# Performance work log

Measured on AMD Instinct MI355X. Metric: run time of the kernel, lower is better.

Reference implementation:

```python
import jax, jax.numpy as jnp
import numpy as np

D = 1024
D_H = 64

def setup_inputs() -> dict:
    key = jax.random.key(0)
    kx, kq, kk, kv = jax.random.split(key, 4)
    B, T = 4, 4096
    x = jax.random.normal(kx, (B, T, D), dtype=jnp.float32)
    # nn.Linear(d, d_H, bias=False) weights, stored as [d, d_H] (already transposed)
    s = 1.0 / np.sqrt(D)
    Wq = jax.random.uniform(kq, (D, D_H), dtype=jnp.float32, minval=-s, maxval=s)
    Wk = jax.random.uniform(kk, (D, D_H), dtype=jnp.float32, minval=-s, maxval=s)
    Wv = jax.random.uniform(kv, (D, D_H), dtype=jnp.float32, minval=-s, maxval=s)
    return {"x": x, "Wq": Wq, "Wk": Wk, "Wv": Wv}

def reference(x, Wq, Wk, Wv):
    B, T, d = x.shape
    Q = jnp.einsum('btd,dh->bth', x, Wq)
    K = jnp.einsum('btd,dh->bth', x, Wk)
    V = jnp.einsum('btd,dh->bth', x, Wv)
    # NOTE: original scales by self.d ** -0.5 (model dim), not d_H
    scores = jnp.einsum('bqh,bkh->bqk', Q, K) * (d ** -0.5)
    causal = jnp.tril(jnp.ones((T, T), dtype=bool))  # [T, T]
    scores = jnp.where(causal, scores, -jnp.inf)
    attn = jax.nn.softmax(scores, axis=-1)
    return jnp.einsum('bqk,bkh->bqh', attn, V)
```

## Files before the change

### kernel.cpp

```cpp
#include <hip/hip_runtime.h>
#include <hip/hip_bf16.h>

#define D_MODEL 1024
#define D_HEAD  64
#define T_SEQ   4096
#define NB      4
#define NROWS   (NB * T_SEQ)
#define SPLIT   8

typedef float f32x4 __attribute__((ext_vector_type(4)));
typedef __bf16 bf16x8 __attribute__((ext_vector_type(8)));
typedef unsigned short u16;
typedef unsigned u32x2 __attribute__((ext_vector_type(2)));
typedef unsigned u32x4 __attribute__((ext_vector_type(4)));

__device__ inline unsigned pk_bf16(float a, float b) {
    unsigned ua = __builtin_bit_cast(unsigned, a);
    unsigned ub = __builtin_bit_cast(unsigned, b);
    ua = (ua + 0x7FFFu + ((ua >> 16) & 1u)) >> 16;
    ub = (ub + 0x7FFFu + ((ub >> 16) & 1u)) >> 16;
    return ua | (ub << 16);
}
__device__ inline u16 bf16r(float a) {
    unsigned ua = __builtin_bit_cast(unsigned, a);
    return (u16)((ua + 0x7FFFu + ((ua >> 16) & 1u)) >> 16);
}

__global__ __launch_bounds__(256) void packw_kernel(
    const float* __restrict__ Wq, const float* __restrict__ Wk,
    const float* __restrict__ Wv, unsigned* __restrict__ Wpk)
{
    const int id = blockIdx.x * 256 + threadIdx.x;
    const int kb = id / 192;
    const int n  = id - kb * 192;
    const int sel = n >> 6, col = n & 63;
    const float* W = sel == 0 ? Wq : (sel == 1 ? Wk : Wv);
    float f[8];
#pragma unroll
    for (int j = 0; j < 8; ++j) f[j] = W[(kb * 8 + j) * 64 + col];
    uint4 o;
    o.x = pk_bf16(f[0], f[1]); o.y = pk_bf16(f[2], f[3]);
    o.z = pk_bf16(f[4], f[5]); o.w = pk_bf16(f[6], f[7]);
    *(uint4*)(Wpk + (size_t)id * 4) = o;
}

__global__ __launch_bounds__(256) void qkv_kernel(
    const float* __restrict__ x, const unsigned* __restrict__ Wpk,
    u16* __restrict__ Qbf, u16* __restrict__ Kbf, u16* __restrict__ Vt)
{
    __shared__ __align__(16) unsigned Xs[2][16 * 68];
    __shared__ __align__(16) u16 Vbuf[64 * 16];

    const int tid  = threadIdx.x;
    const int w    = tid >> 6;
    const int lane = tid & 63;
    const int nl   = lane & 15;
    const int quad = lane >> 4;
    const long row0 = (long)blockIdx.x * 16;

    const int srow = tid >> 5;
    const int scol = (tid & 31) * 4;

    f32x4 acc[3] = {};

    f32x4 nx[2];
#pragma unroll
    for (int p = 0; p < 2; ++p)
        nx[p] = *(const f32x4*)(x + (row0 + p * 8 + srow) * D_MODEL + scol);

    for (int ch = 0; ch < 8; ++ch) {
        const int buf = ch & 1;
#pragma unroll
        for (int p = 0; p < 2; ++p) {
            uint2 pk2;
            pk2.x = pk_bf16(nx[p][0], nx[p][1]);
            pk2.y = pk_bf16(nx[p][2], nx[p][3]);
            *(uint2*)&Xs[buf][(p * 8 + srow) * 68 + (scol >> 1)] = pk2;
        }
        __syncthreads();
        if (ch < 7) {
#pragma unroll
            for (int p = 0; p < 2; ++p)
                nx[p] = *(const f32x4*)(x + (row0 + p * 8 + srow) * D_MODEL
                                          + (ch + 1) * 128 + scol);
        }
#pragma unroll
        for (int kk = 0; kk < 4; ++kk) {
            const bf16x8 a0 = __builtin_bit_cast(bf16x8,
                *(const uint4*)&Xs[buf][nl * 68 + kk * 16 + quad * 4]);
            const unsigned* wb = Wpk + (size_t)(ch * 16 + kk * 4 + quad) * 768
                                     + (w * 48 + nl) * 4;
#pragma unroll
            for (int t = 0; t < 3; ++t) {
                const bf16x8 b = __builtin_bit_cast(bf16x8, *(const uint4*)(wb + t * 64));
                acc[t] = __builtin_amdgcn_mfma_f32_16x16x32_bf16(a0, b, acc[t], 0, 0, 0);
            }
        }
    }
    __syncthreads();

    const float QSCALE = 0.04508422f;
#pragma unroll
    for (int t = 0; t < 3; ++t) {
        const int n0c = w * 48 + t * 16;
        const int sel = n0c >> 6;
        const int col = (n0c & 63) + nl;
        if (sel == 0) {
#pragma unroll
            for (int reg = 0; reg < 4; ++reg)
                Qbf[(row0 + quad * 4 + reg) * D_HEAD + col] =
                    bf16r(acc[t][reg] * QSCALE);
        } else if (sel == 1) {
#pragma unroll
            for (int reg = 0; reg < 4; ++reg)
                Kbf[(row0 + quad * 4 + reg) * D_HEAD + col] =
                    bf16r(acc[t][reg]);
        } else {
            uint2 p2;
            p2.x = pk_bf16(acc[t][0], acc[t][1]);
            p2.y = pk_bf16(acc[t][2], acc[t][3]);
            *(uint2*)&Vbuf[col * 16 + quad * 4] = p2;
        }
    }
    __syncthreads();
    {
        const int dim  = tid >> 2;
        const int tseg = (tid & 3) * 4;
        const long bb   = row0 >> 12;
        const int tpos0 = (int)(row0 & 4095);
        const uint2 v = *(const uint2*)&Vbuf[dim * 16 + tseg];
        *(uint2*)&Vt[((bb * 64 + dim) << 12) + tpos0 + tseg] = v;
    }
}

__global__ __launch_bounds__(256, 3) void attn_kernel(
    const u16* __restrict__ Qbf, const u16* __restrict__ Kbf,
    const u16* __restrict__ Vt, u16* __restrict__ Po16, float* __restrict__ Pl)
{
    __shared__ __align__(16) u16 Pbuf[4][2][16 * 64];

    const int tid   = threadIdx.x;
    const int w     = tid >> 6;
    const int lane  = tid & 63;
    const int nl    = lane & 15;
    const int quad  = lane >> 4;
    const int gid   = blockIdx.x;
    const int b     = gid & 3;
    const int idx   = gid >> 2;
    const int half  = idx & 1;
    const int pair  = idx >> 1;
    const int sp    = half * 4 + w;

    const u16* Kb = Kbf + (size_t)b * T_SEQ * D_HEAD;
    const u16* Vb = Vt  + (size_t)b * D_HEAD * T_SEQ;

    const int tileA = 127 - pair;
    const int tileB = pair;
    const int nA = (tileA * 32 + 95) >> 6;
    const int nB = (tileB * 32 + 95) >> 6;
    const int cntA = (nA - sp + 7) >> 3;
    const int ktB0 = sp + SPLIT * cntA - nA;
    const int cntB = (ktB0 < nB) ? ((nB - ktB0 + 7) >> 3) : 0;

#define COMPUTEKV(kt_) do {                                                          \
    const int _k0 = (kt_) << 6;                                                      \
    uint4 buf[4][2];                                                                 \
    _Pragma("unroll") for (int t = 0; t < 4; ++t) {                                  \
        const u16* kp = Kb + (size_t)(_k0 + t * 16 + nl) * D_HEAD + quad * 8;        \
        buf[t][0] = *(const uint4*)kp;                                               \
        buf[t][1] = *(const uint4*)(kp + 32);                                        \
    }                                                                                \
    f32x4 S[2][4];                                                                   \
    _Pragma("unroll") for (int m = 0; m < 2; ++m)                                    \
    _Pragma("unroll") for (int t = 0; t < 4; ++t) {                                  \
        f32x4 z = {};                                                                \
        z = __builtin_amdgcn_mfma_f32_16x16x32_bf16(qf[m][0],                        \
                __builtin_bit_cast(bf16x8, buf[t][0]), z, 0, 0, 0);                  \
        S[m][t] = __builtin_amdgcn_mfma_f32_16x16x32_bf16(qf[m][1],                  \
                __builtin_bit_cast(bf16x8, buf[t][1]), z, 0, 0, 0);                  \
    }                                                                                \
    uint4 vbuf[4][2];               \
    _Pragma("unroll") for (int t = 0; t < 4; ++t) {                                  \
        const u16* vp = Vb + (size_t)(t * 16 + nl) * T_SEQ + _k0 + quad * 8;         \
        vbuf[t][0] = *(const uint4*)vp;                                              \
        vbuf[t][1] = *(const uint4*)(vp + 32);                                       \
    }                                                                                \
    _Pragma("unroll") for (int m = 0; m < 2; ++m) {                                  \
        const int _qb = wq0 + m * 16;                                                \
        if (_k0 + 63 > _qb) {                                                        \
            _Pragma("unroll") for (int t = 0; t < 4; ++t)                            \
            _Pragma("unroll") for (int reg = 0; reg < 4; ++reg)                      \
                if (_k0 + t * 16 + nl > _qb + quad * 4 + reg)                        \
                    S[m][t][reg] = -INFINITY;                                        \
        }                                                                            \
        _Pragma("unroll") for (int t = 0; t < 4; ++t)                                \
        _Pragma("unroll") for (int reg = 0; reg < 4; ++reg)                          \
            S[m][t][reg] = exp2f(S[m][t][reg]);                                      \
        _Pragma("unroll") for (int reg = 0; reg < 4; ++reg)                          \
            l[m][reg] += (S[m][0][reg] + S[m][1][reg])                               \
                       + (S[m][2][reg] + S[m][3][reg]);                              \
        u16* pb = Pbuf[w][m];                                                        \
        _Pragma("unroll") for (int t = 0; t < 4; ++t) {                              \
            const int g = 2 * t + (nl >> 3);                                         \
            _Pragma("unroll") for (int reg = 0; reg < 4; ++reg) {                    \
                const int q = quad * 4 + reg;                                        \
                pb[q * 64 + ((g ^ (q & 7)) * 8) + (nl & 7)] = bf16r(S[m][t][reg]);   \
            }                                                                        \
        }                                                                            \
    }                                                                                \
    _Pragma("unroll") for (int m = 0; m < 2; ++m) {                                  \
        const u16* pb = Pbuf[w][m];                                                  \
        const bf16x8 pf0 = __builtin_bit_cast(bf16x8,                                \
            *(const uint4*)&pb[nl * 64 + ((quad ^ (nl & 7)) * 8)]);                  \
        const bf16x8 pf1 = __builtin_bit_cast(bf16x8,                                \
            *(const uint4*)&pb[nl * 64 + (((4 + quad) ^ (nl & 7)) * 8)]);            \
        _Pragma("unroll") for (int t = 0; t < 4; ++t) {                              \
            Ot[m][t] = __builtin_amdgcn_mfma_f32_16x16x32_bf16(pf0,                  \
                        __builtin_bit_cast(bf16x8, vbuf[t][0]), Ot[m][t], 0, 0, 0);  \
            Ot[m][t] = __builtin_amdgcn_mfma_f32_16x16x32_bf16(pf1,                  \
                        __builtin_bit_cast(bf16x8, vbuf[t][1]), Ot[m][t], 0, 0, 0);  \
        }                                                                            \
    }                                                                                \
} while (0)

    auto runTile = [&](const int tile, const int kt0, const int cnt) {
        const int wq0 = tile * 32;

        bf16x8 qf[2][2];
#pragma unroll
        for (int m = 0; m < 2; ++m) {
            const u16* qp = Qbf + ((size_t)b * T_SEQ + wq0 + m * 16 + nl) * D_HEAD + quad * 8;
            qf[m][0] = __builtin_bit_cast(bf16x8, *(const uint4*)qp);
            qf[m][1] = __builtin_bit_cast(bf16x8, *(const uint4*)(qp + 32));
        }

        f32x4 Ot[2][4] = {};
        float l[2][4] = {{0.f,0.f,0.f,0.f},{0.f,0.f,0.f,0.f}};

        int kt = kt0;
        for (int i = 0; i < cnt; ++i, kt += SPLIT)
            COMPUTEKV(kt);

#pragma unroll
        for (int m = 0; m < 2; ++m) {
#pragma unroll
            for (int reg = 0; reg < 4; ++reg) {
                float s = l[m][reg];
                s += __shfl_xor(s, 1);
                s += __shfl_xor(s, 2);
                s += __shfl_xor(s, 4);
                s += __shfl_xor(s, 8);
                l[m][reg] = s;
            }
            const int strip = tile * 2 + m;
            const int bs = b * 256 + strip;
            u16* po = Po16 + ((size_t)sp * 1024 + bs) * 1024;
#pragma unroll
            for (int t = 0; t < 4; ++t) {
                u32x2 p2;
                p2[0] = pk_bf16(Ot[m][t][0], Ot[m][t][1]);
                p2[1] = pk_bf16(Ot[m][t][2], Ot[m][t][3]);
                __builtin_nontemporal_store(p2, (u32x2*)&po[(t * 16 + nl) * 16 + quad * 4]);
            }
            if (nl == 0) {
                const size_t gr = (size_t)b * T_SEQ + wq0 + m * 16;
#pragma unroll
                for (int reg = 0; reg < 4; ++reg)
                    __builtin_nontemporal_store(l[m][reg],
                        &Pl[(size_t)sp * NROWS + gr + quad * 4 + reg]);
            }
        }
    };

    runTile(tileA, sp,   cntA);
    runTile(tileB, ktB0, cntB);

#undef COMPUTEKV
}

__global__ __launch_bounds__(256) void reduce_kernel(
    const u16* __restrict__ Po16, const float* __restrict__ Pl,
    float* __restrict__ O)
{
    __shared__ float part[4][16][64];
    __shared__ float lsum[4][16];
    __shared__ float linv[16];
    const int tid = threadIdx.x;
    const int w   = tid >> 6;
    const int c   = tid & 63;
    const int bs  = blockIdx.x;
    const int b   = bs >> 8, strip = bs & 255;
    const size_t gr = (size_t)b * T_SEQ + strip * 16;

    float v[16] = {};
    float ls = 0.f;
#pragma unroll
    for (int i = 0; i < 2; ++i) {
        const int sp = w + i * 4;
        const u16* p = Po16 + ((size_t)sp * 1024 + bs) * 1024 + c * 16;
        const u32x4 x0 = __builtin_nontemporal_load((const u32x4*)p);
        const u32x4 x1 = __builtin_nontemporal_load((const u32x4*)p + 1);
        const unsigned uu[8] = {x0[0], x0[1], x0[2], x0[3], x1[0], x1[1], x1[2], x1[3]};
#pragma unroll
        for (int j = 0; j < 8; ++j) {
            v[2*j]   += __builtin_bit_cast(float, uu[j] << 16);
            v[2*j+1] += __builtin_bit_cast(float, uu[j] & 0xFFFF0000u);
        }
        if (c < 16) ls += Pl[(size_t)sp * NROWS + gr + c];
    }
#pragma unroll
    for (int r = 0; r < 16; ++r) part[w][r][c] = v[r];
    if (c < 16) lsum[w][c] = ls;
    __syncthreads();
    if (tid < 16)
        linv[tid] = 1.0f / (lsum[0][tid] + lsum[1][tid] + lsum[2][tid] + lsum[3][tid]);
    __syncthreads();
#pragma unroll
    for (int j = 0; j < 4; ++j) {
        const int r = w + j * 4;
        const float s = (part[0][r][c] + part[1][r][c]) + (part[2][r][c] + part[3][r][c]);
        O[(gr + r) * D_HEAD + c] = s * linv[r];
    }
}

extern "C" void kernel_launch(void* const* d_in, const int* in_sizes, int n_in,
                              void* d_out, int out_size, void* d_ws, size_t ws_size,
                              hipStream_t stream) {
    const float* x  = (const float*)d_in[0];
    const float* Wq = (const float*)d_in[1];
    const float* Wk = (const float*)d_in[2];
    const float* Wv = (const float*)d_in[3];
    float* out = (float*)d_out;

    const size_t rows = NROWS;
    u16* Qbf = (u16*)d_ws;
    u16* Kbf = Qbf + rows * D_HEAD;
    u16* Vt  = Kbf + rows * D_HEAD;
    unsigned* Wpk = (unsigned*)(Vt + rows * D_HEAD);
    u16* Po16 = (u16*)(Wpk + 128 * 192 * 4);
    float* Pl = (float*)(Po16 + (size_t)SPLIT * rows * D_HEAD);

    hipLaunchKernelGGL(packw_kernel, dim3(96), dim3(256), 0, stream,
                       Wq, Wk, Wv, Wpk);
    hipLaunchKernelGGL(qkv_kernel, dim3(rows / 16), dim3(256), 0, stream,
                       x, Wpk, Qbf, Kbf, Vt);
    hipLaunchKernelGGL(attn_kernel, dim3(512), dim3(256), 0, stream,
                       Qbf, Kbf, Vt, Po16, Pl);
    hipLaunchKernelGGL(reduce_kernel, dim3(NB * 256), dim3(64 * 4), 0, stream,
                       Po16, Pl, out);
}
```

Measured before the change: 159.7 us.

## Share K/V tiles across warps via async LDS staging; widen QKV projection tile

The attention kernel now gives each block a 128-query block where all four warps work on the same split index. K and V tiles are staged once per block into swizzled, double-buffered shared memory with global_load_lds and reused by all warps, instead of each warp reading its own tiles from global memory. Occupancy hint drops to 2 blocks per CU to make room for the larger LDS use. The QKV projection kernel processes 32 rows per block so each weight fragment feeds two MFMAs, and the V transpose store is widened to 16 bytes. The cost is block-wide barriers every K step and lower occupancy.

```diff
diff --git a/kernel.cpp b/kernel.cpp
--- a/kernel.cpp
+++ b/kernel.cpp
@@ -24,6 +24,12 @@
 __device__ inline u16 bf16r(float a) {
     unsigned ua = __builtin_bit_cast(unsigned, a);
     return (u16)((ua + 0x7FFFu + ((ua >> 16) & 1u)) >> 16);
+}
+
+__device__ inline void gload_lds16(const void* g, void* l) {
+    __builtin_amdgcn_global_load_lds(
+        (const __attribute__((address_space(1))) void*)g,
+        (__attribute__((address_space(3))) void*)l, 16, 0, 0);
 }
 
 __global__ __launch_bounds__(256) void packw_kernel(
@@ -48,52 +54,55 @@
     const float* __restrict__ x, const unsigned* __restrict__ Wpk,
     u16* __restrict__ Qbf, u16* __restrict__ Kbf, u16* __restrict__ Vt)
 {
-    __shared__ __align__(16) unsigned Xs[2][16 * 68];
-    __shared__ __align__(16) u16 Vbuf[64 * 16];
+    __shared__ __align__(16) unsigned Xs[2][32 * 68];
+    __shared__ __align__(16) u16 Vbuf[64 * 32];
 
     const int tid  = threadIdx.x;
     const int w    = tid >> 6;
     const int lane = tid & 63;
     const int nl   = lane & 15;
     const int quad = lane >> 4;
-    const long row0 = (long)blockIdx.x * 16;
+    const long row0 = (long)blockIdx.x * 32;
 
     const int srow = tid >> 5;
     const int scol = (tid & 31) * 4;
 
-    f32x4 acc[3] = {};
-
-    f32x4 nx[2];
-#pragma unroll
-    for (int p = 0; p < 2; ++p)
-        nx[p] = *(const f32x4*)(x + (row0 + p * 8 + srow) * D_MODEL + scol);
+    f32x4 acc[2][3] = {};
+
+    float4 nx[4];
+#pragma unroll
+    for (int p = 0; p < 4; ++p)
+        nx[p] = *(const float4*)(x + (row0 + p * 8 + srow) * D_MODEL + scol);
 
     for (int ch = 0; ch < 8; ++ch) {
         const int buf = ch & 1;
 #pragma unroll
-        for (int p = 0; p < 2; ++p) {
+        for (int p = 0; p < 4; ++p) {
             uint2 pk2;
-            pk2.x = pk_bf16(nx[p][0], nx[p][1]);
-            pk2.y = pk_bf16(nx[p][2], nx[p][3]);
+            pk2.x = pk_bf16(nx[p].x, nx[p].y);
+            pk2.y = pk_bf16(nx[p].z, nx[p].w);
             *(uint2*)&Xs[buf][(p * 8 + srow) * 68 + (scol >> 1)] = pk2;
         }
         __syncthreads();
         if (ch < 7) {
 #pragma unroll
-            for (int p = 0; p < 2; ++p)
-                nx[p] = *(const f32x4*)(x + (row0 + p * 8 + srow) * D_MODEL
-                                          + (ch + 1) * 128 + scol);
+            for (int p = 0; p < 4; ++p)
+                nx[p] = *(const float4*)(x + (row0 + p * 8 + srow) * D_MODEL
+                                           + (ch + 1) * 128 + scol);
         }
 #pragma unroll
         for (int kk = 0; kk < 4; ++kk) {
             const bf16x8 a0 = __builtin_bit_cast(bf16x8,
                 *(const uint4*)&Xs[buf][nl * 68 + kk * 16 + quad * 4]);
+            const bf16x8 a1 = __builtin_bit_cast(bf16x8,
+                *(const uint4*)&Xs[buf][(16 + nl) * 68 + kk * 16 + quad * 4]);
             const unsigned* wb = Wpk + (size_t)(ch * 16 + kk * 4 + quad) * 768
                                      + (w * 48 + nl) * 4;
 #pragma unroll
             for (int t = 0; t < 3; ++t) {
                 const bf16x8 b = __builtin_bit_cast(bf16x8, *(const uint4*)(wb + t * 64));
-                acc[t] = __builtin_amdgcn_mfma_f32_16x16x32_bf16(a0, b, acc[t], 0, 0, 0);
+                acc[0][t] = __builtin_amdgcn_mfma_f32_16x16x32_bf16(a0, b, acc[0][t], 0, 0, 0);
+                acc[1][t] = __builtin_amdgcn_mfma_f32_16x16x32_bf16(a1, b, acc[1][t], 0, 0, 0);
             }
         }
     }
@@ -105,38 +114,43 @@
         const int n0c = w * 48 + t * 16;
         const int sel = n0c >> 6;
         const int col = (n0c & 63) + nl;
-        if (sel == 0) {
-#pragma unroll
-            for (int reg = 0; reg < 4; ++reg)
-                Qbf[(row0 + quad * 4 + reg) * D_HEAD + col] =
-                    bf16r(acc[t][reg] * QSCALE);
-        } else if (sel == 1) {
-#pragma unroll
-            for (int reg = 0; reg < 4; ++reg)
-                Kbf[(row0 + quad * 4 + reg) * D_HEAD + col] =
-                    bf16r(acc[t][reg]);
-        } else {
-            uint2 p2;
-            p2.x = pk_bf16(acc[t][0], acc[t][1]);
-            p2.y = pk_bf16(acc[t][2], acc[t][3]);
-            *(uint2*)&Vbuf[col * 16 + quad * 4] = p2;
+#pragma unroll
+        for (int m = 0; m < 2; ++m) {
+            if (sel == 0) {
+#pragma unroll
+                for (int reg = 0; reg < 4; ++reg)
+                    Qbf[(row0 + m * 16 + quad * 4 + reg) * D_HEAD + col] =
+                        bf16r(acc[m][t][reg] * QSCALE);
+            } else if (sel == 1) {
+#pragma unroll
+                for (int reg = 0; reg < 4; ++reg)
+                    Kbf[(row0 + m * 16 + quad * 4 + reg) * D_HEAD + col] =
+                        bf16r(acc[m][t][reg]);
+            } else {
+                uint2 p2;
+                p2.x = pk_bf16(acc[m][t][0], acc[m][t][1]);
+                p2.y = pk_bf16(acc[m][t][2], acc[m][t][3]);
+                *(uint2*)&Vbuf[col * 32 + m * 16 + quad * 4] = p2;
+            }
         }
     }
     __syncthreads();
     {
         const int dim  = tid >> 2;
-        const int tseg = (tid & 3) * 4;
+        const int tseg = (tid & 3) * 8;
         const long bb   = row0 >> 12;
         const int tpos0 = (int)(row0 & 4095);
-        const uint2 v = *(const uint2*)&Vbuf[dim * 16 + tseg];
-        *(uint2*)&Vt[((bb * 64 + dim) << 12) + tpos0 + tseg] = v;
-    }
-}
-
-__global__ __launch_bounds__(256, 3) void attn_kernel(
+        const uint4 v = *(const uint4*)&Vbuf[dim * 32 + tseg];
+        *(uint4*)&Vt[((bb * 64 + dim) << 12) + tpos0 + tseg] = v;
+    }
+}
+
+__global__ __launch_bounds__(256, 2) void attn_kernel(
     const u16* __restrict__ Qbf, const u16* __restrict__ Kbf,
     const u16* __restrict__ Vt, u16* __restrict__ Po16, float* __restrict__ Pl)
 {
+    __shared__ __align__(16) u16 Kls[2][4096];
+    __shared__ __align__(16) u16 Vls[2][4096];
     __shared__ __align__(16) u16 Pbuf[4][2][16 * 64];
 
     const int tid   = threadIdx.x;
@@ -147,28 +161,41 @@
     const int gid   = blockIdx.x;
     const int b     = gid & 3;
     const int idx   = gid >> 2;
-    const int half  = idx & 1;
-    const int pair  = idx >> 1;
-    const int sp    = half * 4 + w;
+    const int sp    = idx & 7;
+    const int pair  = idx >> 3;
 
     const u16* Kb = Kbf + (size_t)b * T_SEQ * D_HEAD;
     const u16* Vb = Vt  + (size_t)b * D_HEAD * T_SEQ;
 
-    const int tileA = 127 - pair;
-    const int tileB = pair;
-    const int nA = (tileA * 32 + 95) >> 6;
-    const int nB = (tileB * 32 + 95) >> 6;
+    const int qbA = 31 - pair;
+    const int qbB = pair;
+    const int nA = 2 * qbA + 2;
+    const int nB = 2 * qbB + 2;
     const int cntA = (nA - sp + 7) >> 3;
     const int ktB0 = sp + SPLIT * cntA - nA;
     const int cntB = (ktB0 < nB) ? ((nB - ktB0 + 7) >> 3) : 0;
 
-#define COMPUTEKV(kt_) do {                                                          \
+    const int swz   = ((lane & 7) ^ ((lane >> 3) & 7)) * 8;
+    const int stgk  = ((lane >> 3) << 6) + swz;
+    const int stgv  = ((lane >> 3) << 12) + swz;
+    const int offh0 = nl * 64 + ((quad ^ (nl & 7)) << 3);
+    const int offh1 = nl * 64 + (((quad + 4) ^ (nl & 7)) << 3);
+
+#define STAGE(cur_, kt_) do {                                                        \
+    const int _s0 = (kt_) << 6;                                                      \
+    _Pragma("unroll") for (int jj = 0; jj < 2; ++jj) {                               \
+        const int j = w * 2 + jj;                                                    \
+        gload_lds16(Kb + (size_t)(_s0 + 8 * j) * 64 + stgk, &Kls[cur_][j * 512]);    \
+        gload_lds16(Vb + (size_t)(8 * j) * 4096 + _s0 + stgv, &Vls[cur_][j * 512]);  \
+    }                                                                                \
+} while (0)
+
+#define COMPUTEKV(cur_, kt_) do {                                                    \
     const int _k0 = (kt_) << 6;                                                      \
     uint4 buf[4][2];                                                                 \
     _Pragma("unroll") for (int t = 0; t < 4; ++t) {                                  \
-        const u16* kp = Kb + (size_t)(_k0 + t * 16 + nl) * D_HEAD + quad * 8;        \
-        buf[t][0] = *(const uint4*)kp;                                               \
-        buf[t][1] = *(const uint4*)(kp + 32);                                        \
+        buf[t][0] = *(const uint4*)&Kls[cur_][t * 1024 + offh0];                     \
+        buf[t][1] = *(const uint4*)&Kls[cur_][t * 1024 + offh1];                     \
     }                                                                                \
     f32x4 S[2][4];                                                                   \
     _Pragma("unroll") for (int m = 0; m < 2; ++m)                                    \
@@ -179,11 +206,10 @@
         S[m][t] = __builtin_amdgcn_mfma_f32_16x16x32_bf16(qf[m][1],                  \
                 __builtin_bit_cast(bf16x8, buf[t][1]), z, 0, 0, 0);                  \
     }                                                                                \
-    uint4 vbuf[4][2];               \
+    uint4 vbuf[4][2];                                                                \
     _Pragma("unroll") for (int t = 0; t < 4; ++t) {                                  \
-        const u16* vp = Vb + (size_t)(t * 16 + nl) * T_SEQ + _k0 + quad * 8;         \
-        vbuf[t][0] = *(const uint4*)vp;                                              \
-        vbuf[t][1] = *(const uint4*)(vp + 32);                                       \
+        vbuf[t][0] = *(const uint4*)&Vls[cur_][t * 1024 + offh0];                    \
+        vbuf[t][1] = *(const uint4*)&Vls[cur_][t * 1024 + offh1];                    \
     }                                                                                \
     _Pragma("unroll") for (int m = 0; m < 2; ++m) {                                  \
         const int _qb = wq0 + m * 16;                                                \
@@ -223,8 +249,8 @@
     }                                                                                \
 } while (0)
 
-    auto runTile = [&](const int tile, const int kt0, const int cnt) {
-        const int wq0 = tile * 32;
+    auto runTile = [&](const int qb, const int kt0, const int cnt) {
+        const int wq0 = qb * 128 + w * 32;
 
         bf16x8 qf[2][2];
 #pragma unroll
@@ -238,8 +264,13 @@
         float l[2][4] = {{0.f,0.f,0.f,0.f},{0.f,0.f,0.f,0.f}};
 
         int kt = kt0;
-        for (int i = 0; i < cnt; ++i, kt += SPLIT)
-            COMPUTEKV(kt);
+        if (cnt > 0) STAGE(0, kt);
+        __syncthreads();
+        for (int i = 0; i < cnt; ++i, kt += SPLIT) {
+            if (i + 1 < cnt) STAGE((i + 1) & 1, kt + SPLIT);
+            COMPUTEKV(i & 1, kt);
+            __syncthreads();
+        }
 
 #pragma unroll
         for (int m = 0; m < 2; ++m) {
@@ -252,7 +283,7 @@
                 s += __shfl_xor(s, 8);
                 l[m][reg] = s;
             }
-            const int strip = tile * 2 + m;
+            const int strip = qb * 8 + w * 2 + m;
             const int bs = b * 256 + strip;
             u16* po = Po16 + ((size_t)sp * 1024 + bs) * 1024;
 #pragma unroll
@@ -263,7 +294,7 @@
                 __builtin_nontemporal_store(p2, (u32x2*)&po[(t * 16 + nl) * 16 + quad * 4]);
             }
             if (nl == 0) {
-                const size_t gr = (size_t)b * T_SEQ + wq0 + m * 16;
+                const size_t gr = (size_t)b * T_SEQ + qb * 128 + w * 32 + m * 16;
 #pragma unroll
                 for (int reg = 0; reg < 4; ++reg)
                     __builtin_nontemporal_store(l[m][reg],
@@ -272,9 +303,10 @@
         }
     };
 
-    runTile(tileA, sp,   cntA);
-    runTile(tileB, ktB0, cntB);
-
+    runTile(qbA, sp,   cntA);
+    runTile(qbB, ktB0, cntB);
+
+#undef STAGE
 #undef COMPUTEKV
 }
 
@@ -342,7 +374,7 @@
 
     hipLaunchKernelGGL(packw_kernel, dim3(96), dim3(256), 0, stream,
                        Wq, Wk, Wv, Wpk);
-    hipLaunchKernelGGL(qkv_kernel, dim3(rows / 16), dim3(256), 0, stream,
+    hipLaunchKernelGGL(qkv_kernel, dim3(rows / 32), dim3(256), 0, stream,
                        x, Wpk, Qbf, Kbf, Vt);
     hipLaunchKernelGGL(attn_kernel, dim3(512), dim3(256), 0, stream,
                        Qbf, Kbf, Vt, Po16, Pl);
```

Result: faster. 140.3 us (-12.1%).
